# Kernel tuning notes

Hardware: AMD Instinct MI355X
Metric: run time of the kernel (lower is better)

Reference implementation:

```python
import jax, jax.numpy as jnp
import numpy as np
import math

N, H, V, K = 8192, 1024, 50257, 4096

def setup_inputs() -> dict:
    key = jax.random.key(0)
    k_in, k_tgt, k_noise, k_w, k_up = jax.random.split(key, 5)
    inp = jax.random.normal(k_in, (N, H), dtype=jnp.float32)
    target = jax.random.randint(k_tgt, (N,), 0, V)
    noise = jax.random.randint(k_noise, (K,), 0, V)  # alias-multinomial draw, fixed here
    stdv = 1.0 / math.sqrt(H)
    weight = jax.random.uniform(k_w, (V, H), dtype=jnp.float32, minval=-stdv, maxval=stdv)
    bias = jnp.full((V,), -math.log(V), dtype=jnp.float32)
    up = jax.random.uniform(k_up, (V,), dtype=jnp.float32, minval=1e-6, maxval=1.0)
    unigram_prob = up / jnp.sum(up)
    return {"input": inp, "weight": weight, "bias": bias,
            "unigram_prob": unigram_prob, "target": target, "noise": noise}

def reference(input, weight, bias, unigram_prob, target, noise):
    # 'train' mode of linear_nce
    w_target = weight[target]                      # [N, H] gather
    b_target = bias[target]                        # [N]
    pmt = jnp.exp(jnp.sum(input * w_target, axis=1) + b_target)   # [N]
    pnt = unigram_prob[target]                     # [N]
    w_noise = weight[noise]                        # [K, H] gather
    b_noise = bias[noise]                          # [K]
    pmn = jnp.exp(jnp.einsum('nh,kh->nk', input, w_noise) + b_noise)  # [N, K]
    pnn = jnp.broadcast_to(unigram_prob[noise][None, :], (input.shape[0], noise.shape[0]))  # [N, K]
    return (pmt, pnt, pmn, pnn)
```

## Files before the change

### kernel.cpp

```cpp
#include <hip/hip_runtime.h>
#include <hip/hip_bf16.h>

#define NROWS 8192
#define HDIM  1024
#define VDIM  50257
#define KNOISE 4096

typedef short  bf16x8 __attribute__((ext_vector_type(8)));
typedef float  f32x4  __attribute__((ext_vector_type(4)));

__device__ __forceinline__ unsigned short f2bf(float x) {
    union { float f; unsigned int u; } v; v.f = x;
    unsigned int r = (v.u + 0x7fffu + ((v.u >> 16) & 1u)) >> 16;
    return (unsigned short)r;
}

__global__ void conv_input_kernel(const float* __restrict__ in,
                                  unsigned short* __restrict__ out) {
    int idx = blockIdx.x * blockDim.x + threadIdx.x;
    const float4* in4 = (const float4*)in;
    float4 v = in4[idx];
    ushort4 o;
    o.x = f2bf(v.x); o.y = f2bf(v.y); o.z = f2bf(v.z); o.w = f2bf(v.w);
    ((ushort4*)out)[idx] = o;
}

__global__ void gather_noise_kernel(const float* __restrict__ weight,
                                    const float* __restrict__ bias,
                                    const float* __restrict__ unigram,
                                    const int* __restrict__ noise,
                                    unsigned short* __restrict__ wn,
                                    float* __restrict__ bn,
                                    float* __restrict__ un) {
    int r = blockIdx.x;
    int idx = noise[r];
    const float4* src = (const float4*)(weight + (size_t)idx * HDIM);
    ushort4* dst = (ushort4*)(wn + (size_t)r * HDIM);
    int t = threadIdx.x;
    float4 v = src[t];
    ushort4 o;
    o.x = f2bf(v.x); o.y = f2bf(v.y); o.z = f2bf(v.z); o.w = f2bf(v.w);
    dst[t] = o;
    if (t == 0) { bn[r] = bias[idx]; un[r] = unigram[idx]; }
}

__global__ void pmt_kernel(const float* __restrict__ in,
                           const float* __restrict__ weight,
                           const float* __restrict__ bias,
                           const float* __restrict__ unigram,
                           const int* __restrict__ target,
                           float* __restrict__ out_pmt,
                           float* __restrict__ out_pnt) {
    int row = blockIdx.x;
    int t   = target[row];
    int tid = threadIdx.x;
    const float4* a4 = (const float4*)(in + (size_t)row * HDIM);
    const float4* w4 = (const float4*)(weight + (size_t)t * HDIM);
    float4 a = a4[tid];
    float4 w = w4[tid];
    float s = a.x * w.x + a.y * w.y + a.z * w.z + a.w * w.w;
    #pragma unroll
    for (int off = 32; off > 0; off >>= 1) s += __shfl_down(s, off);
    __shared__ float red[4];
    if ((tid & 63) == 0) red[tid >> 6] = s;
    __syncthreads();
    if (tid == 0) {
        float tot = red[0] + red[1] + red[2] + red[3];
        out_pmt[row] = expf(tot + bias[t]);
        out_pnt[row] = unigram[t];
    }
}

#define BM 128
#define BN 128
#define BK 32

__global__ __launch_bounds__(256) void gemm_nce_kernel(
        const unsigned short* __restrict__ A,
        const unsigned short* __restrict__ Bt,
        const float* __restrict__ bn,
        const float* __restrict__ un,
        float* __restrict__ pmn,
        float* __restrict__ pnn) {
    __shared__ unsigned short As[BM * BK];
    __shared__ unsigned short Bs[BN * BK];

    const int tid  = threadIdx.x;
    const int lane = tid & 63;
    const int wave = tid >> 6;
    const int wm = wave & 1;
    const int wn = wave >> 1;
    const int row0 = blockIdx.x * BM;
    const int col0 = blockIdx.y * BN;

    const int r = lane & 15;
    const int q = lane >> 4;

    f32x4 acc[4][4];
    #pragma unroll
    for (int mi = 0; mi < 4; mi++)
        #pragma unroll
        for (int ni = 0; ni < 4; ni++)
            acc[mi][ni] = (f32x4){0.f, 0.f, 0.f, 0.f};

    const int c0  = tid;
    const int c1  = tid + 256;
    const int rr0 = c0 >> 2, cc0 = (c0 & 3) * 8;
    const int rr1 = c1 >> 2, cc1 = (c1 & 3) * 8;

    for (int k0 = 0; k0 < HDIM; k0 += BK) {
        *(uint4*)(&As[rr0 * BK + cc0]) = *(const uint4*)(&A[(size_t)(row0 + rr0) * HDIM + k0 + cc0]);
        *(uint4*)(&As[rr1 * BK + cc1]) = *(const uint4*)(&A[(size_t)(row0 + rr1) * HDIM + k0 + cc1]);
        *(uint4*)(&Bs[rr0 * BK + cc0]) = *(const uint4*)(&Bt[(size_t)(col0 + rr0) * HDIM + k0 + cc0]);
        *(uint4*)(&Bs[rr1 * BK + cc1]) = *(const uint4*)(&Bt[(size_t)(col0 + rr1) * HDIM + k0 + cc1]);
        __syncthreads();

        bf16x8 af[4], bfr[4];
        #pragma unroll
        for (int mi = 0; mi < 4; mi++)
            af[mi] = *(const bf16x8*)(&As[(wm * 64 + mi * 16 + r) * BK + q * 8]);
        #pragma unroll
        for (int ni = 0; ni < 4; ni++)
            bfr[ni] = *(const bf16x8*)(&Bs[(wn * 64 + ni * 16 + r) * BK + q * 8]);

        #pragma unroll
        for (int mi = 0; mi < 4; mi++)
            #pragma unroll
            for (int ni = 0; ni < 4; ni++)
                acc[mi][ni] = __builtin_amdgcn_mfma_f32_16x16x32_bf16(af[mi], bfr[ni], acc[mi][ni], 0, 0, 0);

        __syncthreads();
    }

    float bnv[4], unv[4];
    #pragma unroll
    for (int ni = 0; ni < 4; ni++) {
        int cg = col0 + wn * 64 + ni * 16 + r;
        bnv[ni] = bn[cg];
        unv[ni] = un[cg];
    }
    #pragma unroll
    for (int mi = 0; mi < 4; mi++) {
        int rg0 = row0 + wm * 64 + mi * 16 + q * 4;
        #pragma unroll
        for (int ni = 0; ni < 4; ni++) {
            int cg = col0 + wn * 64 + ni * 16 + r;
            #pragma unroll
            for (int j = 0; j < 4; j++) {
                size_t off = (size_t)(rg0 + j) * KNOISE + cg;
                pmn[off] = __expf(acc[mi][ni][j] + bnv[ni]);
                pnn[off] = unv[ni];
            }
        }
    }
}

extern "C" void kernel_launch(void* const* d_in, const int* in_sizes, int n_in,
                              void* d_out, int out_size, void* d_ws, size_t ws_size,
                              hipStream_t stream) {
    const float* input   = (const float*)d_in[0];
    const float* weight  = (const float*)d_in[1];
    const float* bias    = (const float*)d_in[2];
    const float* unigram = (const float*)d_in[3];
    const int*   target  = (const int*)d_in[4];
    const int*   noise   = (const int*)d_in[5];

    unsigned short* in_bf = (unsigned short*)d_ws;
    unsigned short* wn_bf = in_bf + (size_t)NROWS * HDIM;
    float* bn = (float*)(wn_bf + (size_t)KNOISE * HDIM);
    float* un = bn + KNOISE;

    float* out = (float*)d_out;
    float* o_pmt = out;
    float* o_pnt = out + NROWS;
    float* o_pmn = out + 2 * NROWS;
    float* o_pnn = o_pmn + (size_t)NROWS * KNOISE;

    conv_input_kernel<<<(NROWS * HDIM / 4) / 256, 256, 0, stream>>>(input, in_bf);
    gather_noise_kernel<<<KNOISE, 256, 0, stream>>>(weight, bias, unigram, noise, wn_bf, bn, un);
    pmt_kernel<<<NROWS, 256, 0, stream>>>(input, weight, bias, unigram, target, o_pmt, o_pnt);

    dim3 grid(NROWS / BM, KNOISE / BN);
    gemm_nce_kernel<<<grid, 256, 0, stream>>>(in_bf, wn_bf, bn, un, o_pmn, o_pnn);
}
```

Before: 525.2 us.

## Fuse prep kernels, use direct global-to-LDS loads, stage epilogue through LDS

Merges the input conversion, noise gather and target dot-product kernels into one launch, so the input is read once and two launches go away. The GEMM main loop now loads tiles with global_load_lds, skipping the trip through registers. The epilogue writes exp results into a per-wave LDS scratch region and reads them back so pmn can be stored as row-contiguous float4, and pnn is written as float4 broadcasts. Together these target the write-bound output path (about 256MB), with the LDS round trip and the waitcnt-based synchronisation as added cost and risk.

```diff
diff --git a/kernel.cpp b/kernel.cpp
--- a/kernel.cpp
+++ b/kernel.cpp
@@ -15,65 +15,62 @@
     return (unsigned short)r;
 }
 
-__global__ void conv_input_kernel(const float* __restrict__ in,
-                                  unsigned short* __restrict__ out) {
-    int idx = blockIdx.x * blockDim.x + threadIdx.x;
-    const float4* in4 = (const float4*)in;
-    float4 v = in4[idx];
-    ushort4 o;
-    o.x = f2bf(v.x); o.y = f2bf(v.y); o.z = f2bf(v.z); o.w = f2bf(v.w);
-    ((ushort4*)out)[idx] = o;
-}
-
-__global__ void gather_noise_kernel(const float* __restrict__ weight,
-                                    const float* __restrict__ bias,
-                                    const float* __restrict__ unigram,
-                                    const int* __restrict__ noise,
-                                    unsigned short* __restrict__ wn,
-                                    float* __restrict__ bn,
-                                    float* __restrict__ un) {
-    int r = blockIdx.x;
-    int idx = noise[r];
-    const float4* src = (const float4*)(weight + (size_t)idx * HDIM);
-    ushort4* dst = (ushort4*)(wn + (size_t)r * HDIM);
-    int t = threadIdx.x;
-    float4 v = src[t];
-    ushort4 o;
-    o.x = f2bf(v.x); o.y = f2bf(v.y); o.z = f2bf(v.z); o.w = f2bf(v.w);
-    dst[t] = o;
-    if (t == 0) { bn[r] = bias[idx]; un[r] = unigram[idx]; }
-}
-
-__global__ void pmt_kernel(const float* __restrict__ in,
-                           const float* __restrict__ weight,
-                           const float* __restrict__ bias,
-                           const float* __restrict__ unigram,
-                           const int* __restrict__ target,
-                           float* __restrict__ out_pmt,
-                           float* __restrict__ out_pnt) {
-    int row = blockIdx.x;
-    int t   = target[row];
-    int tid = threadIdx.x;
-    const float4* a4 = (const float4*)(in + (size_t)row * HDIM);
-    const float4* w4 = (const float4*)(weight + (size_t)t * HDIM);
-    float4 a = a4[tid];
-    float4 w = w4[tid];
-    float s = a.x * w.x + a.y * w.y + a.z * w.z + a.w * w.w;
-    #pragma unroll
-    for (int off = 32; off > 0; off >>= 1) s += __shfl_down(s, off);
-    __shared__ float red[4];
-    if ((tid & 63) == 0) red[tid >> 6] = s;
-    __syncthreads();
-    if (tid == 0) {
-        float tot = red[0] + red[1] + red[2] + red[3];
-        out_pmt[row] = expf(tot + bias[t]);
-        out_pnt[row] = unigram[t];
+__device__ __forceinline__ void gload16(const void* g, void* l) {
+    __builtin_amdgcn_global_load_lds(
+        (const __attribute__((address_space(1))) void*)g,
+        (__attribute__((address_space(3))) void*)l, 16, 0, 0);
+}
+
+__global__ __launch_bounds__(256) void prep_kernel(
+        const float* __restrict__ input,
+        const float* __restrict__ weight,
+        const float* __restrict__ bias,
+        const float* __restrict__ unigram,
+        const int* __restrict__ target,
+        const int* __restrict__ noise,
+        unsigned short* __restrict__ in_bf,
+        unsigned short* __restrict__ wn_bf,
+        float* __restrict__ bn,
+        float* __restrict__ un,
+        float* __restrict__ out_pmt,
+        float* __restrict__ out_pnt) {
+    const int tid = threadIdx.x;
+    if (blockIdx.x < NROWS) {
+        const int row = blockIdx.x;
+        const int t = target[row];
+        float4 a = ((const float4*)(input + (size_t)row * HDIM))[tid];
+        ushort4 o;
+        o.x = f2bf(a.x); o.y = f2bf(a.y); o.z = f2bf(a.z); o.w = f2bf(a.w);
+        ((ushort4*)(in_bf + (size_t)row * HDIM))[tid] = o;
+        float4 w = ((const float4*)(weight + (size_t)t * HDIM))[tid];
+        float s = a.x * w.x + a.y * w.y + a.z * w.z + a.w * w.w;
+        #pragma unroll
+        for (int off = 32; off > 0; off >>= 1) s += __shfl_down(s, off);
+        __shared__ float red[4];
+        if ((tid & 63) == 0) red[tid >> 6] = s;
+        __syncthreads();
+        if (tid == 0) {
+            float tot = red[0] + red[1] + red[2] + red[3];
+            out_pmt[row] = expf(tot + bias[t]);
+            out_pnt[row] = unigram[t];
+        }
+    } else {
+        const int r = blockIdx.x - NROWS;
+        const int idx = noise[r];
+        float4 v = ((const float4*)(weight + (size_t)idx * HDIM))[tid];
+        ushort4 o;
+        o.x = f2bf(v.x); o.y = f2bf(v.y); o.z = f2bf(v.z); o.w = f2bf(v.w);
+        ((ushort4*)(wn_bf + (size_t)r * HDIM))[tid] = o;
+        if (tid == 0) { bn[r] = bias[idx]; un[r] = unigram[idx]; }
     }
 }
 
 #define BM 128
 #define BN 128
 #define BK 32
+#define EPS_LD 68
+#define EPS_WAVE (16 * EPS_LD)
+#define SMEM_BYTES (4 * EPS_WAVE * 4)
 
 __global__ __launch_bounds__(256) void gemm_nce_kernel(
         const unsigned short* __restrict__ A,
@@ -82,8 +79,9 @@
         const float* __restrict__ un,
         float* __restrict__ pmn,
         float* __restrict__ pnn) {
-    __shared__ unsigned short As[BM * BK];
-    __shared__ unsigned short Bs[BN * BK];
+    __shared__ char smem[SMEM_BYTES];
+    unsigned short* As = (unsigned short*)smem;
+    unsigned short* Bs = (unsigned short*)(smem + BM * BK * 2);
 
     const int tid  = threadIdx.x;
     const int lane = tid & 63;
@@ -103,16 +101,22 @@
         for (int ni = 0; ni < 4; ni++)
             acc[mi][ni] = (f32x4){0.f, 0.f, 0.f, 0.f};
 
-    const int c0  = tid;
-    const int c1  = tid + 256;
-    const int rr0 = c0 >> 2, cc0 = (c0 & 3) * 8;
-    const int rr1 = c1 >> 2, cc1 = (c1 & 3) * 8;
+    const int ch0 = wave * 2;
+    const int ch1 = wave * 2 + 1;
+    const int lr = lane >> 2;
+    const int lc = (lane & 3) * 8;
+    const unsigned short* aT = A  + (size_t)row0 * HDIM;
+    const unsigned short* bT = Bt + (size_t)col0 * HDIM;
+    const unsigned short* ga0 = aT + (size_t)(ch0 * 16 + lr) * HDIM + lc;
+    const unsigned short* ga1 = aT + (size_t)(ch1 * 16 + lr) * HDIM + lc;
+    const unsigned short* gb0 = bT + (size_t)(ch0 * 16 + lr) * HDIM + lc;
+    const unsigned short* gb1 = bT + (size_t)(ch1 * 16 + lr) * HDIM + lc;
 
     for (int k0 = 0; k0 < HDIM; k0 += BK) {
-        *(uint4*)(&As[rr0 * BK + cc0]) = *(const uint4*)(&A[(size_t)(row0 + rr0) * HDIM + k0 + cc0]);
-        *(uint4*)(&As[rr1 * BK + cc1]) = *(const uint4*)(&A[(size_t)(row0 + rr1) * HDIM + k0 + cc1]);
-        *(uint4*)(&Bs[rr0 * BK + cc0]) = *(const uint4*)(&Bt[(size_t)(col0 + rr0) * HDIM + k0 + cc0]);
-        *(uint4*)(&Bs[rr1 * BK + cc1]) = *(const uint4*)(&Bt[(size_t)(col0 + rr1) * HDIM + k0 + cc1]);
+        gload16(ga0 + k0, &As[ch0 * 512]);
+        gload16(ga1 + k0, &As[ch1 * 512]);
+        gload16(gb0 + k0, &Bs[ch0 * 512]);
+        gload16(gb1 + k0, &Bs[ch1 * 512]);
         __syncthreads();
 
         bf16x8 af[4], bfr[4];
@@ -132,26 +136,39 @@
         __syncthreads();
     }
 
-    float bnv[4], unv[4];
-    #pragma unroll
-    for (int ni = 0; ni < 4; ni++) {
-        int cg = col0 + wn * 64 + ni * 16 + r;
-        bnv[ni] = bn[cg];
-        unv[ni] = un[cg];
-    }
+    float* eps = (float*)smem + wave * EPS_WAVE;
+
+    float bnv[4];
+    #pragma unroll
+    for (int ni = 0; ni < 4; ni++)
+        bnv[ni] = bn[col0 + wn * 64 + ni * 16 + r];
+
+    const int rrd = lane >> 4;
+    const int crd = (lane & 15) * 4;
+    float4 unv4 = *(const float4*)&un[col0 + wn * 64 + crd];
+
     #pragma unroll
     for (int mi = 0; mi < 4; mi++) {
-        int rg0 = row0 + wm * 64 + mi * 16 + q * 4;
-        #pragma unroll
-        for (int ni = 0; ni < 4; ni++) {
-            int cg = col0 + wn * 64 + ni * 16 + r;
+        #pragma unroll
+        for (int ni = 0; ni < 4; ni++)
             #pragma unroll
-            for (int j = 0; j < 4; j++) {
-                size_t off = (size_t)(rg0 + j) * KNOISE + cg;
-                pmn[off] = __expf(acc[mi][ni][j] + bnv[ni]);
-                pnn[off] = unv[ni];
-            }
+            for (int j = 0; j < 4; j++)
+                eps[(q * 4 + j) * EPS_LD + ni * 16 + r] = __expf(acc[mi][ni][j] + bnv[ni]);
+        __builtin_amdgcn_s_waitcnt(0);
+        #pragma unroll
+        for (int j = 0; j < 4; j++) {
+            float4 v = *(float4*)&eps[(rrd * 4 + j) * EPS_LD + crd];
+            size_t off = (size_t)(row0 + wm * 64 + mi * 16 + rrd * 4 + j) * KNOISE
+                       + col0 + wn * 64 + crd;
+            *(float4*)&pmn[off] = v;
         }
+    }
+
+    #pragma unroll
+    for (int t = 0; t < 16; t++) {
+        int rr = rrd + 4 * t;
+        size_t off = (size_t)(row0 + wm * 64 + rr) * KNOISE + col0 + wn * 64 + crd;
+        *(float4*)&pnn[off] = unv4;
     }
 }
 
@@ -176,9 +193,9 @@
     float* o_pmn = out + 2 * NROWS;
     float* o_pnn = o_pmn + (size_t)NROWS * KNOISE;
 
-    conv_input_kernel<<<(NROWS * HDIM / 4) / 256, 256, 0, stream>>>(input, in_bf);
-    gather_noise_kernel<<<KNOISE, 256, 0, stream>>>(weight, bias, unigram, noise, wn_bf, bn, un);
-    pmt_kernel<<<NROWS, 256, 0, stream>>>(input, weight, bias, unigram, target, o_pmt, o_pnt);
+    prep_kernel<<<NROWS + KNOISE, 256, 0, stream>>>(
+        input, weight, bias, unigram, target, noise,
+        in_bf, wn_bf, bn, un, o_pmt, o_pnt);
 
     dim3 grid(NROWS / BM, KNOISE / BN);
     gemm_nce_kernel<<<grid, 256, 0, stream>>>(in_bf, wn_bf, bn, un, o_pmn, o_pnn);
```

Result: faster. 476.6 us (-9.2%).
